# Optimization experiments

Measured on AMD Instinct MI355X. Metric: run time of the kernel, lower is better.

## Reference

```python
import jax, jax.numpy as jnp
import numpy as np

ACTION_DIM = 7
CHUNK_SIZE = 4
INPUT_DIM = ACTION_DIM * CHUNK_SIZE  # 28
HIDDEN = 128
LATENT = 64
NUM_CODES = 512
COMMITMENT_COST = 0.25
BATCH = 262144


def setup_inputs() -> dict:
    key = jax.random.key(0)
    ks = jax.random.split(key, 10)

    def lin_init(k, fan_in, fan_out):
        # torch nn.Linear default: U(-1/sqrt(fan_in), 1/sqrt(fan_in)) for W and b
        bound = 1.0 / np.sqrt(fan_in)
        kw, kb = jax.random.split(k)
        W = jax.random.uniform(kw, (fan_in, fan_out), jnp.float32, -bound, bound)
        b = jax.random.uniform(kb, (fan_out,), jnp.float32, -bound, bound)
        return W, b

    x = jax.random.normal(ks[0], (BATCH, INPUT_DIM), jnp.float32)
    enc_w1, enc_b1 = lin_init(ks[1], INPUT_DIM, HIDDEN)
    enc_w2, enc_b2 = lin_init(ks[2], HIDDEN, LATENT)
    codebook = jax.random.uniform(
        ks[3], (NUM_CODES, LATENT), jnp.float32, -1.0 / NUM_CODES, 1.0 / NUM_CODES
    )
    dec_w1, dec_b1 = lin_init(ks[4], LATENT, HIDDEN)
    dec_w2, dec_b2 = lin_init(ks[5], HIDDEN, INPUT_DIM)
    return {
        "x": x,
        "enc_w1": enc_w1, "enc_b1": enc_b1,
        "enc_w2": enc_w2, "enc_b2": enc_b2,
        "codebook": codebook,
        "dec_w1": dec_w1, "dec_b1": dec_b1,
        "dec_w2": dec_w2, "dec_b2": dec_b2,
    }


def reference(x, enc_w1, enc_b1, enc_w2, enc_b2, codebook,
              dec_w1, dec_b1, dec_w2, dec_b2):
    sg = jax.lax.stop_gradient
    # Encoder: Linear -> ReLU -> Linear
    h = jax.nn.relu(x @ enc_w1 + enc_b1)          # (B, 128)
    z = h @ enc_w2 + enc_b2                       # (B, 64)
    # Nearest-code lookup: ||z||^2 + ||e||^2 - 2 z.e
    z2 = jnp.sum(z * z, axis=1, keepdims=True)    # (B, 1)
    e2 = jnp.sum(codebook * codebook, axis=1)     # (C,)
    ze = z @ codebook.T                           # (B, C) dominant intermediate
    distances = z2 + e2 - 2.0 * ze
    indices = jnp.argmin(distances, axis=1)       # (B,)
    quantized = codebook[indices]                 # (B, 64) gather
    # VQ losses
    codebook_loss = jnp.mean((sg(z) - quantized) ** 2)
    commitment_loss = jnp.mean((z - sg(quantized)) ** 2)
    vq_loss = codebook_loss + COMMITMENT_COST * commitment_loss
    # Straight-through estimator
    z_q = z + sg(quantized - z)
    # Decoder
    hd = jax.nn.relu(z_q @ dec_w1 + dec_b1)       # (B, 128)
    recon = hd @ dec_w2 + dec_b2                  # (B, 28)
    recon_loss = jnp.mean((recon - x) ** 2)
    return recon, recon_loss, vq_loss
```

## Files before the change

kernel.cpp:

```cpp
#include <hip/hip_runtime.h>

#define BATCH   262144
#define IN_DIM  28
#define HID     128
#define LAT     64
#define NCODES  512
#define NBLK    256
#define WVS     16
#define NWAVE   (NBLK * WVS)

#define S1 40
#define S2 136
#define SC 72
#define O_LW1 0
#define O_LW2 5120
#define O_LCB 13824
#define O_LD1 50688
#define O_LD2 59904
#define BLOB_SHORTS 64256
#define BLOB_F32    864
#define BLOB_BYTES  (BLOB_SHORTS * 2 + BLOB_F32 * 4)
#define LDS_BYTES   BLOB_BYTES

#define E2_BASE   BLOB_SHORTS
#define B1_BASE   (BLOB_SHORTS + 4096)
#define B2_BASE   (B1_BASE + 128)
#define DB1_BASE  (B2_BASE + 64)
#define DB2_BASE  (DB1_BASE + 128)
#define PREP_END  (DB2_BASE + 32)

typedef short v4s __attribute__((ext_vector_type(4)));
typedef short v8s __attribute__((ext_vector_type(8)));
typedef float v4f __attribute__((ext_vector_type(4)));

union u4v8 { unsigned u[4]; v8s s; };

__device__ __forceinline__ unsigned short f2bf(float f) {
  unsigned u = __float_as_uint(f);
  u += 0x7fffu + ((u >> 16) & 1u);
  return (unsigned short)(u >> 16);
}
__device__ __forceinline__ unsigned pk(float hi, float lo) {
  return __builtin_amdgcn_perm(__float_as_uint(hi), __float_as_uint(lo), 0x07060302u);
}
__device__ __forceinline__ float xf0(unsigned u) { return __uint_as_float(u << 16); }
__device__ __forceinline__ float xf1(unsigned u) { return __uint_as_float(u & 0xFFFF0000u); }

__device__ __forceinline__ v4f mfma32(v8s a, v8s b, v4f c) {
  return __builtin_amdgcn_mfma_f32_16x16x32_bf16(a, b, c, 0, 0, 0);
}

__device__ __forceinline__ v8s rlpk2(v4f h0, v4f h1) {
  u4v8 c;
  c.u[0] = pk(fmaxf(h0[1], 0.f), fmaxf(h0[0], 0.f));
  c.u[1] = pk(fmaxf(h0[3], 0.f), fmaxf(h0[2], 0.f));
  c.u[2] = pk(fmaxf(h1[1], 0.f), fmaxf(h1[0], 0.f));
  c.u[3] = pk(fmaxf(h1[3], 0.f), fmaxf(h1[2], 0.f));
  return c.s;
}
__device__ __forceinline__ v8s zpk2(v4f z0, v4f z1) {
  u4v8 c;
  c.u[0] = pk(z0[1], z0[0]); c.u[1] = pk(z0[3], z0[2]);
  c.u[2] = pk(z1[1], z1[0]); c.u[3] = pk(z1[3], z1[2]);
  return c.s;
}
__device__ __forceinline__ v8s mkv8(unsigned a, unsigned b, unsigned c2, unsigned d) {
  u4v8 c; c.u[0] = a; c.u[1] = b; c.u[2] = c2; c.u[3] = d; return c.s;
}
__device__ __forceinline__ float kpack(float d, unsigned code) {
  return __uint_as_float((__float_as_uint(d) & 0xFFFFFE00u) | code);
}

__global__ __launch_bounds__(256) void vq_prep(
    const float* __restrict__ ew1, const float* __restrict__ eb1,
    const float* __restrict__ ew2, const float* __restrict__ eb2,
    const float* __restrict__ cb,  const float* __restrict__ dw1,
    const float* __restrict__ db1, const float* __restrict__ dw2,
    const float* __restrict__ db2,
    unsigned short* __restrict__ blob) {
  int i = blockIdx.x * 256 + threadIdx.x;
  float* fb = (float*)(blob + BLOB_SHORTS);
  if (i < O_LW2) {
    int row = i / S1, s = i % S1;
    unsigned short v = 0;
    if (s < 32) {
      int q = s >> 3, r2 = s & 7, j = r2 >> 2, e = r2 & 3;
      int k = j * 16 + q * 4 + e;
      if (k < IN_DIM) v = f2bf(ew1[k * HID + row]);
    }
    blob[i] = v;
  } else if (i < O_LCB) {
    int j2 = i - O_LW2; int row = j2 / S2, s = j2 % S2;
    unsigned short v = 0;
    if (s < 128) {
      int q = s >> 5, r2 = s & 31, j = r2 >> 2, e = r2 & 3;
      int k = j * 16 + q * 4 + e;
      v = f2bf(ew2[k * LAT + row]);
    }
    blob[i] = v;
  } else if (i < O_LD1) {
    int j2 = i - O_LCB; int row = j2 / SC, s = j2 % SC;
    unsigned short v = 0;
    if (s < 64) {
      int q = s >> 4, r2 = s & 15, j = r2 >> 2, e = r2 & 3;
      int k = j * 16 + q * 4 + e;
      v = f2bf(-2.0f * cb[row * LAT + k]);
    }
    blob[i] = v;
  } else if (i < O_LD2) {
    int j2 = i - O_LD1; int row = j2 / SC, s = j2 % SC;
    unsigned short v = 0;
    if (s < 64) {
      int q = s >> 4, r2 = s & 15, j = r2 >> 2, e = r2 & 3;
      int k = j * 16 + q * 4 + e;
      v = f2bf(-0.5f * dw1[k * HID + row]);
    }
    blob[i] = v;
  } else if (i < BLOB_SHORTS) {
    int j2 = i - O_LD2; int row = j2 / S2, s = j2 % S2;
    unsigned short v = 0;
    if (s < 128 && row < IN_DIM) {
      int q = s >> 5, r2 = s & 31, j = r2 >> 2, e = r2 & 3;
      int k = j * 16 + q * 4 + e;
      v = f2bf(dw2[k * IN_DIM + row]);
    }
    blob[i] = v;
  } else if (i < B1_BASE) {
    int j = i - E2_BASE;
    int c = j >> 3, l = j & 7;
    const float* p = cb + c * LAT + l * 8;
    float4 a = *(const float4*)p;
    float4 b = *(const float4*)(p + 4);
    float s = a.x * a.x + a.y * a.y + a.z * a.z + a.w * a.w
            + b.x * b.x + b.y * b.y + b.z * b.z + b.w * b.w;
    s += __shfl_xor(s, 1, 64);
    s += __shfl_xor(s, 2, 64);
    s += __shfl_xor(s, 4, 64);
    if (l == 0) fb[c] = s;
  } else if (i < B2_BASE) {
    fb[512 + (i - B1_BASE)] = eb1[i - B1_BASE];
  } else if (i < DB1_BASE) {
    fb[640 + (i - B2_BASE)] = eb2[i - B2_BASE];
  } else if (i < DB2_BASE) {
    fb[704 + (i - DB1_BASE)] = db1[i - DB1_BASE];
  } else if (i < PREP_END) {
    int k = i - DB2_BASE;
    fb[832 + k] = (k < IN_DIM) ? db2[k] : 0.f;
  }
}

__device__ __forceinline__ void s12_pair(
    const unsigned short* __restrict__ L, const float* __restrict__ LF,
    int lm, int quad, v8s bxa, v8s bxb,
    v8s& zfa01, v8s& zfa23, v8s& zfb01, v8s& zfb23,
    float& z2a, float& z2b) {
  const int fw1 = O_LW1 + lm * S1 + quad * 8;
  const int fw2 = O_LW2 + lm * S2 + quad * 32;
  v4f za[4], zb[4];
#pragma unroll
  for (int nt = 0; nt < 4; ++nt) {
    v4f s = *(const v4f*)&LF[640 + nt * 16 + quad * 4];
    za[nt] = s; zb[nt] = s;
  }
#pragma unroll 1
  for (int jp = 0; jp < 4; ++jp) {
    v8s hA, hB;
    {
      v8s w0 = *(const v8s*)&L[fw1 + (2 * jp) * (16 * S1)];
      v4f s0 = *(const v4f*)&LF[512 + (2 * jp) * 16 + quad * 4];
      v8s w1 = *(const v8s*)&L[fw1 + (2 * jp + 1) * (16 * S1)];
      v4f s1 = *(const v4f*)&LF[512 + (2 * jp + 1) * 16 + quad * 4];
      v4f h0a = mfma32(w0, bxa, s0);
      v4f h1a = mfma32(w1, bxa, s1);
      v4f h0b = mfma32(w0, bxb, s0);
      v4f h1b = mfma32(w1, bxb, s1);
      hA = rlpk2(h0a, h1a);
      hB = rlpk2(h0b, h1b);
    }
#pragma unroll
    for (int nt = 0; nt < 4; ++nt) {
      v8s w2 = *(const v8s*)&L[fw2 + nt * (16 * S2) + jp * 8];
      za[nt] = mfma32(w2, hA, za[nt]);
      zb[nt] = mfma32(w2, hB, zb[nt]);
    }
  }
  z2a = za[0][0] * za[0][0] + za[0][1] * za[0][1] + za[0][2] * za[0][2] + za[0][3] * za[0][3]
      + za[1][0] * za[1][0] + za[1][1] * za[1][1] + za[1][2] * za[1][2] + za[1][3] * za[1][3]
      + za[2][0] * za[2][0] + za[2][1] * za[2][1] + za[2][2] * za[2][2] + za[2][3] * za[2][3]
      + za[3][0] * za[3][0] + za[3][1] * za[3][1] + za[3][2] * za[3][2] + za[3][3] * za[3][3];
  z2b = zb[0][0] * zb[0][0] + zb[0][1] * zb[0][1] + zb[0][2] * zb[0][2] + zb[0][3] * zb[0][3]
      + zb[1][0] * zb[1][0] + zb[1][1] * zb[1][1] + zb[1][2] * zb[1][2] + zb[1][3] * zb[1][3]
      + zb[2][0] * zb[2][0] + zb[2][1] * zb[2][1] + zb[2][2] * zb[2][2] + zb[2][3] * zb[2][3]
      + zb[3][0] * zb[3][0] + zb[3][1] * zb[3][1] + zb[3][2] * zb[3][2] + zb[3][3] * zb[3][3];
  zfa01 = zpk2(za[0], za[1]); zfa23 = zpk2(za[2], za[3]);
  zfb01 = zpk2(zb[0], zb[1]); zfb23 = zpk2(zb[2], zb[3]);
}

__device__ __forceinline__ void s56_pair(
    const unsigned short* __restrict__ L, const float* __restrict__ LF,
    int lm, int quad, int codeA, int codeB,
    unsigned xa0, unsigned xa1, unsigned xa2, unsigned xa3,
    unsigned xb0, unsigned xb1, unsigned xb2, unsigned xb3,
    float* __restrict__ orowA, float* __restrict__ orowB, float& racc) {
  const int fd1 = O_LD1 + lm * SC + quad * 16;
  const int fd2 = O_LD2 + lm * S2 + quad * 32;
  const int gA = O_LCB + codeA * SC + quad * 16;
  const int gB = O_LCB + codeB * SC + quad * 16;
  v8s qa0 = *(const v8s*)&L[gA];
  v8s qa1 = *(const v8s*)&L[gA + 8];
  v8s qb0 = *(const v8s*)&L[gB];
  v8s qb1 = *(const v8s*)&L[gB + 8];
  v4f a6a[2], a6b[2];
#pragma unroll
  for (int nt = 0; nt < 2; ++nt) {
    v4f s = *(const v4f*)&LF[832 + nt * 16 + quad * 4];
    a6a[nt] = s; a6b[nt] = s;
  }
#pragma unroll 1
  for (int jp = 0; jp < 4; ++jp) {
    v8s hA, hB;
    {
      int j0 = 2 * jp;
      v8s d00 = *(const v8s*)&L[fd1 + j0 * (16 * SC)];
      v8s d01 = *(const v8s*)&L[fd1 + j0 * (16 * SC) + 8];
      v4f s0 = *(const v4f*)&LF[704 + j0 * 16 + quad * 4];
      v8s d10 = *(const v8s*)&L[fd1 + (j0 + 1) * (16 * SC)];
      v8s d11 = *(const v8s*)&L[fd1 + (j0 + 1) * (16 * SC) + 8];
      v4f s1 = *(const v4f*)&LF[704 + (j0 + 1) * 16 + quad * 4];
      v4f h0 = mfma32(d00, qa0, s0);
      h0 = mfma32(d01, qa1, h0);
      v4f h1 = mfma32(d10, qa0, s1);
      h1 = mfma32(d11, qa1, h1);
      hA = rlpk2(h0, h1);
      h0 = mfma32(d00, qb0, s0);
      h0 = mfma32(d01, qb1, h0);
      h1 = mfma32(d10, qb0, s1);
      h1 = mfma32(d11, qb1, h1);
      hB = rlpk2(h0, h1);
    }
#pragma unroll
    for (int nt = 0; nt < 2; ++nt) {
      v8s w6 = *(const v8s*)&L[fd2 + nt * (16 * S2) + jp * 8];
      a6a[nt] = mfma32(w6, hA, a6a[nt]);
      a6b[nt] = mfma32(w6, hB, a6b[nt]);
    }
  }
  *(float4*)(orowA + quad * 4) = (float4){a6a[0][0], a6a[0][1], a6a[0][2], a6a[0][3]};
  *(float4*)(orowB + quad * 4) = (float4){a6b[0][0], a6b[0][1], a6b[0][2], a6b[0][3]};
  if (quad < 3) {
    *(float4*)(orowA + 16 + quad * 4) = (float4){a6a[1][0], a6a[1][1], a6a[1][2], a6a[1][3]};
    *(float4*)(orowB + 16 + quad * 4) = (float4){a6b[1][0], a6b[1][1], a6b[1][2], a6b[1][3]};
  }
  float d;
  d = a6a[0][0] - xf0(xa0); racc += d * d;
  d = a6a[0][1] - xf1(xa0); racc += d * d;
  d = a6a[0][2] - xf0(xa1); racc += d * d;
  d = a6a[0][3] - xf1(xa1); racc += d * d;
  d = a6a[1][0] - xf0(xa2); racc += d * d;
  d = a6a[1][1] - xf1(xa2); racc += d * d;
  d = a6a[1][2] - xf0(xa3); racc += d * d;
  d = a6a[1][3] - xf1(xa3); racc += d * d;
  d = a6b[0][0] - xf0(xb0); racc += d * d;
  d = a6b[0][1] - xf1(xb0); racc += d * d;
  d = a6b[0][2] - xf0(xb1); racc += d * d;
  d = a6b[0][3] - xf1(xb1); racc += d * d;
  d = a6b[1][0] - xf0(xb2); racc += d * d;
  d = a6b[1][1] - xf1(xb2); racc += d * d;
  d = a6b[1][2] - xf0(xb3); racc += d * d;
  d = a6b[1][3] - xf1(xb3); racc += d * d;
}

__global__ __attribute__((amdgpu_flat_work_group_size(1024, 1024)))
__attribute__((amdgpu_waves_per_eu(4, 4)))
void vq_main(
    const float* __restrict__ x,
    const unsigned short* __restrict__ blob,
    float* __restrict__ out, float* __restrict__ partials) {

  extern __shared__ __align__(16) char smem[];
  const unsigned short* L = (const unsigned short*)smem;
  const float*         LF = (const float*)(smem + BLOB_SHORTS * 2);

  const int tid  = threadIdx.x;
  const int wave = tid >> 6;
  const int lane = tid & 63;
  const int quad = lane >> 4;
  const int lm   = lane & 15;

  {
    const float4* src = (const float4*)blob;
    float4* dst = (float4*)smem;
#pragma unroll
    for (int it = 0; it < 9; ++it) {
      int idx = it * 1024 + tid;
      if (idx < BLOB_BYTES / 16) dst[idx] = src[idx];
    }
  }
  __syncthreads();

  const int rbase = blockIdx.x * 1024 + wave * 64;
  float racc = 0.f, vqacc = 0.f;

#pragma unroll 1
  for (int sw = 0; sw < 2; ++sw) {
    const int r0 = rbase + sw * 32;

    unsigned xa0, xa1, xa2, xa3, xb0, xb1, xb2, xb3;
    {
      const float* xpa = x + (size_t)(r0 + lm) * IN_DIM;
      const float* xpb = x + (size_t)(r0 + 16 + lm) * IN_DIM;
      float4 t = *(const float4*)(xpa + quad * 4);
      xa0 = pk(t.y, t.x); xa1 = pk(t.w, t.z);
      t = (quad < 3) ? *(const float4*)(xpa + 16 + quad * 4) : (float4){0.f, 0.f, 0.f, 0.f};
      xa2 = pk(t.y, t.x); xa3 = pk(t.w, t.z);
      t = *(const float4*)(xpb + quad * 4);
      xb0 = pk(t.y, t.x); xb1 = pk(t.w, t.z);
      t = (quad < 3) ? *(const float4*)(xpb + 16 + quad * 4) : (float4){0.f, 0.f, 0.f, 0.f};
      xb2 = pk(t.y, t.x); xb3 = pk(t.w, t.z);
    }

    v8s zfa01, zfa23, zfb01, zfb23;
    float z2a, z2b;
    s12_pair(L, LF, lm, quad,
             mkv8(xa0, xa1, xa2, xa3), mkv8(xb0, xb1, xb2, xb3),
             zfa01, zfa23, zfb01, zfb23, z2a, z2b);

    const int fcb = O_LCB + lm * SC + quad * 16;
    float bkA = __uint_as_float(0x7f7fffffu);
    float bkB = bkA;
#pragma unroll 2
    for (int ct = 0; ct < 32; ++ct) {
      v8s c0 = *(const v8s*)&L[fcb + ct * (16 * SC)];
      v8s c1 = *(const v8s*)&L[fcb + ct * (16 * SC) + 8];
      v4f sd = *(const v4f*)&LF[ct * 16 + quad * 4];
      v4f dA = mfma32(c0, zfa01, sd);
      dA = mfma32(c1, zfa23, dA);
      v4f dB = mfma32(c0, zfb01, sd);
      dB = mfma32(c1, zfb23, dB);
      unsigned cbase = (unsigned)(ct * 16 + quad * 4);
      bkA = fminf(bkA, fminf(fminf(kpack(dA[0], cbase), kpack(dA[1], cbase + 1)),
                             fminf(kpack(dA[2], cbase + 2), kpack(dA[3], cbase + 3))));
      bkB = fminf(bkB, fminf(fminf(kpack(dB[0], cbase), kpack(dB[1], cbase + 1)),
                             fminf(kpack(dB[2], cbase + 2), kpack(dB[3], cbase + 3))));
    }

#pragma unroll
    for (int off = 16; off < 64; off <<= 1) {
      bkA = fminf(bkA, __shfl_xor(bkA, off, 64));
      bkB = fminf(bkB, __shfl_xor(bkB, off, 64));
      z2a += __shfl_xor(z2a, off, 64);
      z2b += __shfl_xor(z2b, off, 64);
    }
    unsigned ka = __float_as_uint(bkA), kb = __float_as_uint(bkB);
    int codeA = (int)(ka & 511u), codeB = (int)(kb & 511u);
    if (quad == 0)
      vqacc += z2a + __uint_as_float(ka & 0xFFFFFE00u)
             + z2b + __uint_as_float(kb & 0xFFFFFE00u);

    s56_pair(L, LF, lm, quad, codeA, codeB,
             xa0, xa1, xa2, xa3, xb0, xb1, xb2, xb3,
             out + (size_t)(r0 + lm) * IN_DIM,
             out + (size_t)(r0 + 16 + lm) * IN_DIM, racc);
  }

#pragma unroll
  for (int off = 1; off < 64; off <<= 1) {
    racc  += __shfl_xor(racc, off, 64);
    vqacc += __shfl_xor(vqacc, off, 64);
  }
  if (lane == 0) {
    size_t w = (size_t)blockIdx.x * WVS + wave;
    partials[w * 2]     = racc;
    partials[w * 2 + 1] = vqacc;
  }
}

__global__ __launch_bounds__(256) void vq_fin(const float* __restrict__ partials,
                                              float* __restrict__ out) {
  float r = 0.f, v = 0.f;
  for (int i = threadIdx.x; i < NWAVE; i += 256) {
    r += partials[2 * i];
    v += partials[2 * i + 1];
  }
#pragma unroll
  for (int off = 1; off < 64; off <<= 1) {
    r += __shfl_xor(r, off, 64);
    v += __shfl_xor(v, off, 64);
  }
  __shared__ float s[4][2];
  int w = threadIdx.x >> 6;
  if ((threadIdx.x & 63) == 0) { s[w][0] = r; s[w][1] = v; }
  __syncthreads();
  if (threadIdx.x == 0) {
    float R = s[0][0] + s[1][0] + s[2][0] + s[3][0];
    float V = s[0][1] + s[1][1] + s[2][1] + s[3][1];
    out[7340032] = R * (1.0f / 7340032.0f);
    out[7340033] = V * (1.25f / 16777216.0f);
  }
}

extern "C" void kernel_launch(void* const* d_in, const int* in_sizes, int n_in,
                              void* d_out, int out_size, void* d_ws, size_t ws_size,
                              hipStream_t stream) {
  const float* x   = (const float*)d_in[0];
  const float* ew1 = (const float*)d_in[1];
  const float* eb1 = (const float*)d_in[2];
  const float* ew2 = (const float*)d_in[3];
  const float* eb2 = (const float*)d_in[4];
  const float* cb  = (const float*)d_in[5];
  const float* dw1 = (const float*)d_in[6];
  const float* db1 = (const float*)d_in[7];
  const float* dw2 = (const float*)d_in[8];
  const float* db2 = (const float*)d_in[9];

  char* ws = (char*)d_ws;
  unsigned short* blob = (unsigned short*)(ws + 0);
  float* partials = (float*)(ws + 132096);

  float* out = (float*)d_out;

  (void)hipFuncSetAttribute((const void*)vq_main,
                            hipFuncAttributeMaxDynamicSharedMemorySize, LDS_BYTES);

  vq_prep<<<(PREP_END + 255) / 256, 256, 0, stream>>>(
      ew1, eb1, ew2, eb2, cb, dw1, db1, dw2, db2, blob);
  vq_main<<<NBLK, 1024, LDS_BYTES, stream>>>(x, blob, out, partials);
  vq_fin<<<1, 256, 0, stream>>>(partials, out);
}
```

Before: 132.4 us.

## Move codebook out of LDS to global memory, double blocks for occupancy

The bf16 codebook (512x64) is moved from the LDS blob into a separate global buffer read directly by the distance loop and the quantized gather. This shrinks LDS per block from roughly 132KB to about 58KB, which allows multiple 1024-thread blocks per CU. Each wave now processes one 32-row tile instead of two, the grid is doubled, and the waves_per_eu bound is relaxed. The trade-off is that codebook reads in the hot loop now go through the L1/L2 cache instead of LDS.

Measured after the change: 173.4 us. 1.31x slower.

```diff
diff --git a/kernel.cpp b/kernel.cpp
--- a/kernel.cpp
+++ b/kernel.cpp
@@ -5,7 +5,7 @@
 #define HID     128
 #define LAT     64
 #define NCODES  512
-#define NBLK    256
+#define NBLK    512
 #define WVS     16
 #define NWAVE   (NBLK * WVS)
 
@@ -14,16 +14,16 @@
 #define SC 72
 #define O_LW1 0
 #define O_LW2 5120
-#define O_LCB 13824
-#define O_LD1 50688
-#define O_LD2 59904
-#define BLOB_SHORTS 64256
+#define O_LD1 13824
+#define O_LD2 23040
+#define BLOB_SHORTS 27392
 #define BLOB_F32    864
 #define BLOB_BYTES  (BLOB_SHORTS * 2 + BLOB_F32 * 4)
 #define LDS_BYTES   BLOB_BYTES
-
-#define E2_BASE   BLOB_SHORTS
-#define B1_BASE   (BLOB_SHORTS + 4096)
+#define CBG_SHORTS  (NCODES * LAT)
+
+#define E2_BASE   (BLOB_SHORTS + CBG_SHORTS)
+#define B1_BASE   (E2_BASE + 4096)
 #define B2_BASE   (B1_BASE + 128)
 #define DB1_BASE  (B2_BASE + 64)
 #define DB2_BASE  (DB1_BASE + 128)
@@ -77,7 +77,7 @@
     const float* __restrict__ cb,  const float* __restrict__ dw1,
     const float* __restrict__ db1, const float* __restrict__ dw2,
     const float* __restrict__ db2,
-    unsigned short* __restrict__ blob) {
+    unsigned short* __restrict__ blob, unsigned short* __restrict__ cbg) {
   int i = blockIdx.x * 256 + threadIdx.x;
   float* fb = (float*)(blob + BLOB_SHORTS);
   if (i < O_LW2) {
@@ -89,22 +89,13 @@
       if (k < IN_DIM) v = f2bf(ew1[k * HID + row]);
     }
     blob[i] = v;
-  } else if (i < O_LCB) {
+  } else if (i < O_LD1) {
     int j2 = i - O_LW2; int row = j2 / S2, s = j2 % S2;
     unsigned short v = 0;
     if (s < 128) {
       int q = s >> 5, r2 = s & 31, j = r2 >> 2, e = r2 & 3;
       int k = j * 16 + q * 4 + e;
       v = f2bf(ew2[k * LAT + row]);
-    }
-    blob[i] = v;
-  } else if (i < O_LD1) {
-    int j2 = i - O_LCB; int row = j2 / SC, s = j2 % SC;
-    unsigned short v = 0;
-    if (s < 64) {
-      int q = s >> 4, r2 = s & 15, j = r2 >> 2, e = r2 & 3;
-      int k = j * 16 + q * 4 + e;
-      v = f2bf(-2.0f * cb[row * LAT + k]);
     }
     blob[i] = v;
   } else if (i < O_LD2) {
@@ -125,6 +116,12 @@
       v = f2bf(dw2[k * IN_DIM + row]);
     }
     blob[i] = v;
+  } else if (i < E2_BASE) {
+    int j = i - BLOB_SHORTS;
+    int code = j >> 6, s = j & 63;
+    int q = s >> 4, r2 = s & 15, j4 = r2 >> 2, e = r2 & 3;
+    int k = j4 * 16 + q * 4 + e;
+    cbg[j] = f2bf(-2.0f * cb[code * LAT + k]);
   } else if (i < B1_BASE) {
     int j = i - E2_BASE;
     int c = j >> 3, l = j & 7;
@@ -198,18 +195,19 @@
 
 __device__ __forceinline__ void s56_pair(
     const unsigned short* __restrict__ L, const float* __restrict__ LF,
+    const unsigned short* __restrict__ cbg,
     int lm, int quad, int codeA, int codeB,
     unsigned xa0, unsigned xa1, unsigned xa2, unsigned xa3,
     unsigned xb0, unsigned xb1, unsigned xb2, unsigned xb3,
     float* __restrict__ orowA, float* __restrict__ orowB, float& racc) {
   const int fd1 = O_LD1 + lm * SC + quad * 16;
   const int fd2 = O_LD2 + lm * S2 + quad * 32;
-  const int gA = O_LCB + codeA * SC + quad * 16;
-  const int gB = O_LCB + codeB * SC + quad * 16;
-  v8s qa0 = *(const v8s*)&L[gA];
-  v8s qa1 = *(const v8s*)&L[gA + 8];
-  v8s qb0 = *(const v8s*)&L[gB];
-  v8s qb1 = *(const v8s*)&L[gB + 8];
+  const unsigned short* gA = cbg + codeA * LAT + quad * 16;
+  const unsigned short* gB = cbg + codeB * LAT + quad * 16;
+  v8s qa0 = *(const v8s*)gA;
+  v8s qa1 = *(const v8s*)(gA + 8);
+  v8s qb0 = *(const v8s*)gB;
+  v8s qb1 = *(const v8s*)(gB + 8);
   v4f a6a[2], a6b[2];
 #pragma unroll
   for (int nt = 0; nt < 2; ++nt) {
@@ -271,10 +269,11 @@
 }
 
 __global__ __attribute__((amdgpu_flat_work_group_size(1024, 1024)))
-__attribute__((amdgpu_waves_per_eu(4, 4)))
+__attribute__((amdgpu_waves_per_eu(4, 8)))
 void vq_main(
     const float* __restrict__ x,
     const unsigned short* __restrict__ blob,
+    const unsigned short* __restrict__ cbg,
     float* __restrict__ out, float* __restrict__ partials) {
 
   extern __shared__ __align__(16) char smem[];
@@ -291,77 +290,72 @@
     const float4* src = (const float4*)blob;
     float4* dst = (float4*)smem;
 #pragma unroll
-    for (int it = 0; it < 9; ++it) {
+    for (int it = 0; it < 4; ++it) {
       int idx = it * 1024 + tid;
       if (idx < BLOB_BYTES / 16) dst[idx] = src[idx];
     }
   }
   __syncthreads();
 
-  const int rbase = blockIdx.x * 1024 + wave * 64;
+  const int r0 = blockIdx.x * 512 + wave * 32;
   float racc = 0.f, vqacc = 0.f;
 
-#pragma unroll 1
-  for (int sw = 0; sw < 2; ++sw) {
-    const int r0 = rbase + sw * 32;
-
-    unsigned xa0, xa1, xa2, xa3, xb0, xb1, xb2, xb3;
-    {
-      const float* xpa = x + (size_t)(r0 + lm) * IN_DIM;
-      const float* xpb = x + (size_t)(r0 + 16 + lm) * IN_DIM;
-      float4 t = *(const float4*)(xpa + quad * 4);
-      xa0 = pk(t.y, t.x); xa1 = pk(t.w, t.z);
-      t = (quad < 3) ? *(const float4*)(xpa + 16 + quad * 4) : (float4){0.f, 0.f, 0.f, 0.f};
-      xa2 = pk(t.y, t.x); xa3 = pk(t.w, t.z);
-      t = *(const float4*)(xpb + quad * 4);
-      xb0 = pk(t.y, t.x); xb1 = pk(t.w, t.z);
-      t = (quad < 3) ? *(const float4*)(xpb + 16 + quad * 4) : (float4){0.f, 0.f, 0.f, 0.f};
-      xb2 = pk(t.y, t.x); xb3 = pk(t.w, t.z);
-    }
-
-    v8s zfa01, zfa23, zfb01, zfb23;
-    float z2a, z2b;
-    s12_pair(L, LF, lm, quad,
-             mkv8(xa0, xa1, xa2, xa3), mkv8(xb0, xb1, xb2, xb3),
-             zfa01, zfa23, zfb01, zfb23, z2a, z2b);
-
-    const int fcb = O_LCB + lm * SC + quad * 16;
-    float bkA = __uint_as_float(0x7f7fffffu);
-    float bkB = bkA;
+  unsigned xa0, xa1, xa2, xa3, xb0, xb1, xb2, xb3;
+  {
+    const float* xpa = x + (size_t)(r0 + lm) * IN_DIM;
+    const float* xpb = x + (size_t)(r0 + 16 + lm) * IN_DIM;
+    float4 t = *(const float4*)(xpa + quad * 4);
+    xa0 = pk(t.y, t.x); xa1 = pk(t.w, t.z);
+    t = (quad < 3) ? *(const float4*)(xpa + 16 + quad * 4) : (float4){0.f, 0.f, 0.f, 0.f};
+    xa2 = pk(t.y, t.x); xa3 = pk(t.w, t.z);
+    t = *(const float4*)(xpb + quad * 4);
+    xb0 = pk(t.y, t.x); xb1 = pk(t.w, t.z);
+    t = (quad < 3) ? *(const float4*)(xpb + 16 + quad * 4) : (float4){0.f, 0.f, 0.f, 0.f};
+    xb2 = pk(t.y, t.x); xb3 = pk(t.w, t.z);
+  }
+
+  v8s zfa01, zfa23, zfb01, zfb23;
+  float z2a, z2b;
+  s12_pair(L, LF, lm, quad,
+           mkv8(xa0, xa1, xa2, xa3), mkv8(xb0, xb1, xb2, xb3),
+           zfa01, zfa23, zfb01, zfb23, z2a, z2b);
+
+  const unsigned short* cbp = cbg + lm * LAT + quad * 16;
+  float bkA = __uint_as_float(0x7f7fffffu);
+  float bkB = bkA;
 #pragma unroll 2
-    for (int ct = 0; ct < 32; ++ct) {
-      v8s c0 = *(const v8s*)&L[fcb + ct * (16 * SC)];
-      v8s c1 = *(const v8s*)&L[fcb + ct * (16 * SC) + 8];
-      v4f sd = *(const v4f*)&LF[ct * 16 + quad * 4];
-      v4f dA = mfma32(c0, zfa01, sd);
-      dA = mfma32(c1, zfa23, dA);
-      v4f dB = mfma32(c0, zfb01, sd);
-      dB = mfma32(c1, zfb23, dB);
-      unsigned cbase = (unsigned)(ct * 16 + quad * 4);
-      bkA = fminf(bkA, fminf(fminf(kpack(dA[0], cbase), kpack(dA[1], cbase + 1)),
-                             fminf(kpack(dA[2], cbase + 2), kpack(dA[3], cbase + 3))));
-      bkB = fminf(bkB, fminf(fminf(kpack(dB[0], cbase), kpack(dB[1], cbase + 1)),
-                             fminf(kpack(dB[2], cbase + 2), kpack(dB[3], cbase + 3))));
-    }
-
-#pragma unroll
-    for (int off = 16; off < 64; off <<= 1) {
-      bkA = fminf(bkA, __shfl_xor(bkA, off, 64));
-      bkB = fminf(bkB, __shfl_xor(bkB, off, 64));
-      z2a += __shfl_xor(z2a, off, 64);
-      z2b += __shfl_xor(z2b, off, 64);
-    }
-    unsigned ka = __float_as_uint(bkA), kb = __float_as_uint(bkB);
-    int codeA = (int)(ka & 511u), codeB = (int)(kb & 511u);
-    if (quad == 0)
-      vqacc += z2a + __uint_as_float(ka & 0xFFFFFE00u)
-             + z2b + __uint_as_float(kb & 0xFFFFFE00u);
-
-    s56_pair(L, LF, lm, quad, codeA, codeB,
-             xa0, xa1, xa2, xa3, xb0, xb1, xb2, xb3,
-             out + (size_t)(r0 + lm) * IN_DIM,
-             out + (size_t)(r0 + 16 + lm) * IN_DIM, racc);
-  }
+  for (int ct = 0; ct < 32; ++ct) {
+    v8s c0 = *(const v8s*)(cbp + ct * (16 * LAT));
+    v8s c1 = *(const v8s*)(cbp + ct * (16 * LAT) + 8);
+    v4f sd = *(const v4f*)&LF[ct * 16 + quad * 4];
+    v4f dA = mfma32(c0, zfa01, sd);
+    dA = mfma32(c1, zfa23, dA);
+    v4f dB = mfma32(c0, zfb01, sd);
+    dB = mfma32(c1, zfb23, dB);
+    unsigned cbase = (unsigned)(ct * 16 + quad * 4);
+    bkA = fminf(bkA, fminf(fminf(kpack(dA[0], cbase), kpack(dA[1], cbase + 1)),
+                           fminf(kpack(dA[2], cbase + 2), kpack(dA[3], cbase + 3))));
+    bkB = fminf(bkB, fminf(fminf(kpack(dB[0], cbase), kpack(dB[1], cbase + 1)),
+                           fminf(kpack(dB[2], cbase + 2), kpack(dB[3], cbase + 3))));
+  }
+
+#pragma unroll
+  for (int off = 16; off < 64; off <<= 1) {
+    bkA = fminf(bkA, __shfl_xor(bkA, off, 64));
+    bkB = fminf(bkB, __shfl_xor(bkB, off, 64));
+    z2a += __shfl_xor(z2a, off, 64);
+    z2b += __shfl_xor(z2b, off, 64);
+  }
+  unsigned ka = __float_as_uint(bkA), kb = __float_as_uint(bkB);
+  int codeA = (int)(ka & 511u), codeB = (int)(kb & 511u);
+  if (quad == 0)
+    vqacc += z2a + __uint_as_float(ka & 0xFFFFFE00u)
+           + z2b + __uint_as_float(kb & 0xFFFFFE00u);
+
+  s56_pair(L, LF, cbg, lm, quad, codeA, codeB,
+           xa0, xa1, xa2, xa3, xb0, xb1, xb2, xb3,
+           out + (size_t)(r0 + lm) * IN_DIM,
+           out + (size_t)(r0 + 16 + lm) * IN_DIM, racc);
 
 #pragma unroll
   for (int off = 1; off < 64; off <<= 1) {
@@ -415,7 +409,8 @@
 
   char* ws = (char*)d_ws;
   unsigned short* blob = (unsigned short*)(ws + 0);
-  float* partials = (float*)(ws + 132096);
+  unsigned short* cbg  = (unsigned short*)(ws + 58368);
+  float* partials      = (float*)(ws + 58368 + 65536);
 
   float* out = (float*)d_out;
 
@@ -423,7 +418,7 @@
                             hipFuncAttributeMaxDynamicSharedMemorySize, LDS_BYTES);
 
   vq_prep<<<(PREP_END + 255) / 256, 256, 0, stream>>>(
-      ew1, eb1, ew2, eb2, cb, dw1, db1, dw2, db2, blob);
-  vq_main<<<NBLK, 1024, LDS_BYTES, stream>>>(x, blob, out, partials);
+      ew1, eb1, ew2, eb2, cb, dw1, db1, dw2, db2, blob, cbg);
+  vq_main<<<NBLK, 1024, LDS_BYTES, stream>>>(x, blob, cbg, out, partials);
   vq_fin<<<1, 256, 0, stream>>>(partials, out);
 }
```
